# Kernel optimization log

Hardware: AMD Instinct MI355X
Metric: run time of the kernel (lower is better)

Reference implementation:

```python
import jax, jax.numpy as jnp
import numpy as np

WINDOW_SIZE = 11
SIGMA = 1.5
C1 = 0.01 ** 2
C2 = 0.03 ** 2


def _gaussian_window(window_size: int, channel: int) -> jnp.ndarray:
    # 1D gaussian, normalized
    g = jnp.arange(window_size, dtype=jnp.float32) - window_size // 2
    g = jnp.exp(-(g ** 2) / (2.0 * SIGMA ** 2))
    g = g / g.sum()
    w2d = jnp.outer(g, g)  # [K, K]
    # depthwise conv kernel: [C, 1, K, K] in OIHW with feature_group_count=C
    return jnp.broadcast_to(w2d[None, None], (channel, 1, window_size, window_size))


def _depthwise_conv(x: jnp.ndarray, window: jnp.ndarray, channel: int) -> jnp.ndarray:
    pad = WINDOW_SIZE // 2
    return jax.lax.conv_general_dilated(
        x, window,
        window_strides=(1, 1),
        padding=((pad, pad), (pad, pad)),
        dimension_numbers=('NCHW', 'OIHW', 'NCHW'),
        feature_group_count=channel,
    )


def setup_inputs() -> dict:
    key = jax.random.key(0)
    k1, k2 = jax.random.split(key)
    shape = (16, 3, 512, 512)
    img1 = jax.random.uniform(k1, shape, dtype=jnp.float32)
    img2 = jax.random.uniform(k2, shape, dtype=jnp.float32)
    return {"img1": img1, "img2": img2}


def reference(img1, img2):
    channel = img1.shape[1]
    window = _gaussian_window(WINDOW_SIZE, channel).astype(img1.dtype)

    mu1 = _depthwise_conv(img1, window, channel)
    mu2 = _depthwise_conv(img2, window, channel)

    mu1_sq = mu1 * mu1
    mu2_sq = mu2 * mu2
    mu1_mu2 = mu1 * mu2

    sigma1_sq = _depthwise_conv(img1 * img1, window, channel) - mu1_sq
    sigma2_sq = _depthwise_conv(img2 * img2, window, channel) - mu2_sq
    sigma12 = _depthwise_conv(img1 * img2, window, channel) - mu1_mu2

    ssim_map = ((2.0 * mu1_mu2 + C1) * (2.0 * sigma12 + C2)) / (
        (mu1_sq + mu2_sq + C1) * (sigma1_sq + sigma2_sq + C2))

    return 1.0 - ssim_map.mean()
```

## Files before the change

kernel.cpp:

```cpp
#include <hip/hip_runtime.h>

#define IMG_H 512
#define IMG_W 512
#define NPLANES 48
#define N_ELEMS (16 * 3 * 512 * 512)

#define TW 32
#define TH 32
#define NTHREADS 256
#define GX (IMG_W / TW)
#define GY (IMG_H / TH)
#define NBLOCKS (GX * GY * NPLANES)

#define RS4 43

#define C1f 1.0e-4f
#define C2f 9.0e-4f

typedef float v2f __attribute__((ext_vector_type(2)));

__device__ __forceinline__ v2f pkfma(float w, v2f v, v2f acc) {
    v2f wv = {w, w};
    return __builtin_elementwise_fma(wv, v, acc);
}

__global__ void __launch_bounds__(NTHREADS, 7) ssim_main(
    const float* __restrict__ img1, const float* __restrict__ img2,
    float* __restrict__ partials)
{
    __shared__ float4 r[TH * RS4];
    __shared__ float wpart[NTHREADS / 64];

    const int tid = threadIdx.x;

    const int work = (blockIdx.x & 7) * (NBLOCKS / 8) + (blockIdx.x >> 3);
    const int plane = work >> 8;
    const int rem = work & 255;
    const int by = rem >> 4, bx = rem & 15;
    const int tx0 = bx * TW, ty0 = by * TH;
    const float* p1 = img1 + (size_t)plane * IMG_H * IMG_W;
    const float* p2 = img2 + (size_t)plane * IMG_H * IMG_W;

    constexpr float G[11] = {
        0.00102838f, 0.00759876f, 0.03600077f, 0.10936070f, 0.21300553f,
        0.26601173f,
        0.21300553f, 0.10936070f, 0.03600077f, 0.00759876f, 0.00102838f
    };

    if (tid < 168) {
        const int c = tid % 42;
        const int g = tid / 42;
        const int gx = tx0 - 5 + c;
        const int gy0 = ty0 + 8 * g - 5;

        v2f asd[8], ass[8];
#pragma unroll
        for (int k = 0; k < 8; ++k) { asd[k] = (v2f)0.0f; ass[k] = (v2f)0.0f; }

        const bool inter = ((unsigned)gx < IMG_W) & (gy0 >= 0) &
                           (gy0 + 17 < IMG_H);
        if (inter) {
            const float* pa = p1 + (size_t)gy0 * IMG_W + gx;
            const float* pb = p2 + (size_t)gy0 * IMG_W + gx;
#pragma unroll
            for (int j = 0; j < 18; ++j) {
                float a = pa[j * IMG_W];
                float b = pb[j * IMG_W];
                v2f sd; sd.x = a + b; sd.y = a - b;
                v2f sq = sd * sd;
#pragma unroll
                for (int k = 0; k < 8; ++k) {
                    int t = j - k;
                    if (t >= 0 && t < 11) {
                        asd[k] = pkfma(G[t], sd, asd[k]);
                        ass[k] = pkfma(G[t], sq, ass[k]);
                    }
                }
            }
        } else {
            const int cx = min(max(gx, 0), IMG_W - 1);
            const float mx = ((unsigned)gx < IMG_W) ? 1.0f : 0.0f;
#pragma unroll
            for (int j = 0; j < 18; ++j) {
                int gy = gy0 + j;
                int cy = min(max(gy, 0), IMG_H - 1);
                float m = ((unsigned)gy < IMG_H) ? mx : 0.0f;
                size_t off = (size_t)cy * IMG_W + cx;
                float a = p1[off] * m;
                float b = p2[off] * m;
                v2f sd; sd.x = a + b; sd.y = a - b;
                v2f sq = sd * sd;
#pragma unroll
                for (int k = 0; k < 8; ++k) {
                    int t = j - k;
                    if (t >= 0 && t < 11) {
                        asd[k] = pkfma(G[t], sd, asd[k]);
                        ass[k] = pkfma(G[t], sq, ass[k]);
                    }
                }
            }
        }
#pragma unroll
        for (int k = 0; k < 8; ++k)
            r[(8 * g + k) * RS4 + c] =
                make_float4(asd[k].x, asd[k].y, ass[k].x, ass[k].y);
    }
    __syncthreads();

    float local = 0.0f;
    if (tid < 128) {
        const int hy = tid >> 2;
        const int x0 = (tid & 3) * 8;
        v2f osd[8], oss[8];
#pragma unroll
        for (int k = 0; k < 8; ++k) { osd[k] = (v2f)0.0f; oss[k] = (v2f)0.0f; }

#pragma unroll
        for (int j = 0; j < 18; ++j) {
            float4 v = r[hy * RS4 + x0 + j];
            v2f va; va.x = v.x; va.y = v.y;
            v2f vb; vb.x = v.z; vb.y = v.w;
#pragma unroll
            for (int k = 0; k < 8; ++k) {
                int t = j - k;
                if (t >= 0 && t < 11) {
                    osd[k] = pkfma(G[t], va, osd[k]);
                    oss[k] = pkfma(G[t], vb, oss[k]);
                }
            }
        }

#pragma unroll
        for (int k = 0; k < 8; ++k) {
            v2f sd2 = osd[k] * osd[k];
            float cs2 = sd2.x, cd2 = sd2.y;
            float css = oss[k].x, cdd = oss[k].y;
            float mu12 = 0.25f * (cs2 - cd2);
            float musq = 0.50f * (cs2 + cd2);
            float e12  = 0.25f * (css - cdd);
            float esum = 0.50f * (css + cdd);
            float sg12  = e12 - mu12;
            float sgsum = esum - musq;
            float num = (2.0f * mu12 + C1f) * (2.0f * sg12 + C2f);
            float den = (musq + C1f) * (sgsum + C2f);
            local += num * __builtin_amdgcn_rcpf(den);
        }
    }

#pragma unroll
    for (int off = 32; off > 0; off >>= 1) local += __shfl_down(local, off, 64);
    if ((tid & 63) == 0) wpart[tid >> 6] = local;
    __syncthreads();
    if (tid == 0)
        partials[blockIdx.x] = wpart[0] + wpart[1] + wpart[2] + wpart[3];
}

__global__ void ssim_final(const float* __restrict__ partials,
                           float* __restrict__ out)
{
    __shared__ float wp[4];
    const int tid = threadIdx.x;
    const float4* p4 = (const float4*)partials;
    float s = 0.0f;
#pragma unroll
    for (int k = 0; k < 12; ++k) {
        float4 v = p4[tid + k * NTHREADS];
        s += (v.x + v.y) + (v.z + v.w);
    }
#pragma unroll
    for (int off = 32; off > 0; off >>= 1) s += __shfl_down(s, off, 64);
    if ((tid & 63) == 0) wp[tid >> 6] = s;
    __syncthreads();
    if (tid == 0)
        out[0] = 1.0f - (wp[0] + wp[1] + wp[2] + wp[3]) * (1.0f / (float)N_ELEMS);
}

extern "C" void kernel_launch(void* const* d_in, const int* in_sizes, int n_in,
                              void* d_out, int out_size, void* d_ws, size_t ws_size,
                              hipStream_t stream) {
    const float* img1 = (const float*)d_in[0];
    const float* img2 = (const float*)d_in[1];
    float* out = (float*)d_out;
    float* partials = (float*)d_ws;

    ssim_main<<<NBLOCKS, NTHREADS, 0, stream>>>(img1, img2, partials);
    ssim_final<<<1, NTHREADS, 0, stream>>>(partials, out);
}
```

Baseline: 150.2 us.

## Compute separable Gaussian convolutions with bf16 MFMA banded-matrix products

Replaces the scalar packed-FMA separable Gaussian passes with bf16 MFMA 16x16x32 matrix multiplies against banded Gaussian weight matrices. Image sums, differences and their squares are packed to bf16, then run through a horizontal pass. The results go to LDS as transposed bf16, and the vertical pass is a second MFMA. Global loads become vectorized float4 row reads. The aim is to move the convolution arithmetic off the vector ALUs, at the cost of bf16 rounding of inputs, squares and intermediates, which may hurt accuracy of the variance terms.

```diff
diff --git a/kernel.cpp b/kernel.cpp
--- a/kernel.cpp
+++ b/kernel.cpp
@@ -4,152 +4,153 @@
 #define IMG_W 512
 #define NPLANES 48
 #define N_ELEMS (16 * 3 * 512 * 512)
-
-#define TW 32
-#define TH 32
 #define NTHREADS 256
-#define GX (IMG_W / TW)
-#define GY (IMG_H / TH)
-#define NBLOCKS (GX * GY * NPLANES)
-
-#define RS4 43
+#define NBLOCKS 12288
+#define LSTR 56
 
 #define C1f 1.0e-4f
 #define C2f 9.0e-4f
 
-typedef float v2f __attribute__((ext_vector_type(2)));
+typedef float v4f __attribute__((ext_vector_type(4)));
+typedef short v8s __attribute__((ext_vector_type(8)));
 
-__device__ __forceinline__ v2f pkfma(float w, v2f v, v2f acc) {
-    v2f wv = {w, w};
-    return __builtin_elementwise_fma(wv, v, acc);
+__device__ __constant__ float GT[64] = {
+    0,0,0,0,0,0,0,0,0,0,0,0,0,0,0,0,0,0,0,0,0,0,0,0,
+    0.00102838f, 0.00759876f, 0.03600077f, 0.10936070f, 0.21300553f,
+    0.26601173f,
+    0.21300553f, 0.10936070f, 0.03600077f, 0.00759876f, 0.00102838f,
+    0,0,0,0,0,0,0,0,0,0,0,0,0,0,0,0,0,0,0,0,0,0,0,0,0,0,0,0,0
+};
+
+__device__ __forceinline__ unsigned int pk2bf(float x, float y) {
+    unsigned int ax = __float_as_uint(x) + 0x8000u;
+    unsigned int by = __float_as_uint(y) + 0x8000u;
+    return __builtin_amdgcn_perm(by, ax, 0x07060302);
 }
 
-__global__ void __launch_bounds__(NTHREADS, 7) ssim_main(
+__global__ void __launch_bounds__(NTHREADS, 4) ssim_main(
     const float* __restrict__ img1, const float* __restrict__ img2,
     float* __restrict__ partials)
 {
-    __shared__ float4 r[TH * RS4];
-    __shared__ float wpart[NTHREADS / 64];
+    __shared__ short T[128 * LSTR];
+    __shared__ float wpart[4];
 
     const int tid = threadIdx.x;
+    const int lane = tid & 63;
+    const int wv = tid >> 6;
+    const int m = lane & 15;
+    const int qd = lane >> 4;
 
     const int work = (blockIdx.x & 7) * (NBLOCKS / 8) + (blockIdx.x >> 3);
     const int plane = work >> 8;
     const int rem = work & 255;
     const int by = rem >> 4, bx = rem & 15;
-    const int tx0 = bx * TW, ty0 = by * TH;
+    const int tx0 = bx * 32, ty0 = by * 32;
     const float* p1 = img1 + (size_t)plane * IMG_H * IMG_W;
     const float* p2 = img2 + (size_t)plane * IMG_H * IMG_W;
 
-    constexpr float G[11] = {
-        0.00102838f, 0.00759876f, 0.03600077f, 0.10936070f, 0.21300553f,
-        0.26601173f,
-        0.21300553f, 0.10936070f, 0.03600077f, 0.00759876f, 0.00102838f
-    };
+    v8s gX, gY;
+    {
+        union { v8s v; unsigned int u[4]; } uy, ux;
+#pragma unroll
+        for (int i = 0; i < 4; ++i) {
+            int k0 = qd * 8 + 2 * i;
+            uy.u[i] = pk2bf(GT[24 + k0 - m], GT[25 + k0 - m]);
+            ux.u[i] = pk2bf(GT[21 + k0 - m], GT[22 + k0 - m]);
+        }
+        gY = uy.v; gX = ux.v;
+    }
 
-    if (tid < 168) {
-        const int c = tid % 42;
-        const int g = tid / 42;
-        const int gx = tx0 - 5 + c;
-        const int gy0 = ty0 + 8 * g - 5;
+    const bool interior = (bx > 0) & (bx < 15) & (by > 0) & (by < 15);
+    const v4f zero4 = {0.f, 0.f, 0.f, 0.f};
 
-        v2f asd[8], ass[8];
 #pragma unroll
-        for (int k = 0; k < 8; ++k) { asd[k] = (v2f)0.0f; ass[k] = (v2f)0.0f; }
-
-        const bool inter = ((unsigned)gx < IMG_W) & (gy0 >= 0) &
-                           (gy0 + 17 < IMG_H);
-        if (inter) {
-            const float* pa = p1 + (size_t)gy0 * IMG_W + gx;
-            const float* pb = p2 + (size_t)gy0 * IMG_W + gx;
+    for (int cc = 0; cc < 2; ++cc) {
+        int c = wv + 4 * cc;
+        if (c < 6) {
+            const int yg = c >> 1, xoh = c & 1;
+            const int yrow = yg * 16 + m;
+            const int gy = ty0 - 5 + yrow;
+            const int xb = tx0 - 8 + xoh * 16 + qd * 8;
+            float a[8], b[8];
+            if (interior) {
+                const float* pa = p1 + (size_t)gy * IMG_W + xb;
+                const float* pb = p2 + (size_t)gy * IMG_W + xb;
+                *(float4*)&a[0] = *(const float4*)pa;
+                *(float4*)&a[4] = *(const float4*)(pa + 4);
+                *(float4*)&b[0] = *(const float4*)pb;
+                *(float4*)&b[4] = *(const float4*)(pb + 4);
+            } else {
+                const int gyc = min(max(gy, 0), IMG_H - 1);
+                const bool oky = (unsigned)gy < IMG_H;
+                const float* ra = p1 + (size_t)gyc * IMG_W;
+                const float* rb = p2 + (size_t)gyc * IMG_W;
 #pragma unroll
-            for (int j = 0; j < 18; ++j) {
-                float a = pa[j * IMG_W];
-                float b = pb[j * IMG_W];
-                v2f sd; sd.x = a + b; sd.y = a - b;
-                v2f sq = sd * sd;
-#pragma unroll
-                for (int k = 0; k < 8; ++k) {
-                    int t = j - k;
-                    if (t >= 0 && t < 11) {
-                        asd[k] = pkfma(G[t], sd, asd[k]);
-                        ass[k] = pkfma(G[t], sq, ass[k]);
-                    }
+                for (int j = 0; j < 8; ++j) {
+                    int gx = xb + j;
+                    int gxc = min(max(gx, 0), IMG_W - 1);
+                    bool ok = oky && ((unsigned)gx < IMG_W);
+                    a[j] = ok ? ra[gxc] : 0.f;
+                    b[j] = ok ? rb[gxc] : 0.f;
                 }
             }
-        } else {
-            const int cx = min(max(gx, 0), IMG_W - 1);
-            const float mx = ((unsigned)gx < IMG_W) ? 1.0f : 0.0f;
+            union { v8s v; unsigned int u[4]; } fs, fd, fss, fdd;
 #pragma unroll
-            for (int j = 0; j < 18; ++j) {
-                int gy = gy0 + j;
-                int cy = min(max(gy, 0), IMG_H - 1);
-                float m = ((unsigned)gy < IMG_H) ? mx : 0.0f;
-                size_t off = (size_t)cy * IMG_W + cx;
-                float a = p1[off] * m;
-                float b = p2[off] * m;
-                v2f sd; sd.x = a + b; sd.y = a - b;
-                v2f sq = sd * sd;
-#pragma unroll
-                for (int k = 0; k < 8; ++k) {
-                    int t = j - k;
-                    if (t >= 0 && t < 11) {
-                        asd[k] = pkfma(G[t], sd, asd[k]);
-                        ass[k] = pkfma(G[t], sq, ass[k]);
-                    }
-                }
+            for (int i = 0; i < 4; ++i) {
+                float s0 = a[2*i] + b[2*i], s1 = a[2*i+1] + b[2*i+1];
+                float d0 = a[2*i] - b[2*i], d1 = a[2*i+1] - b[2*i+1];
+                fs.u[i]  = pk2bf(s0, s1);
+                fd.u[i]  = pk2bf(d0, d1);
+                fss.u[i] = pk2bf(s0 * s0, s1 * s1);
+                fdd.u[i] = pk2bf(d0 * d0, d1 * d1);
             }
+            v4f t0 = __builtin_amdgcn_mfma_f32_16x16x32_bf16(fs.v,  gX, zero4, 0, 0, 0);
+            v4f t1 = __builtin_amdgcn_mfma_f32_16x16x32_bf16(fd.v,  gX, zero4, 0, 0, 0);
+            v4f t2 = __builtin_amdgcn_mfma_f32_16x16x32_bf16(fss.v, gX, zero4, 0, 0, 0);
+            v4f t3 = __builtin_amdgcn_mfma_f32_16x16x32_bf16(fdd.v, gX, zero4, 0, 0, 0);
+            const int ybase = yg * 16 + qd * 4;
+            const int rbase = xoh * 16 + m;
+            *(uint2*)&T[(0 * 32 + rbase) * LSTR + ybase] =
+                make_uint2(pk2bf(t0[0], t0[1]), pk2bf(t0[2], t0[3]));
+            *(uint2*)&T[(1 * 32 + rbase) * LSTR + ybase] =
+                make_uint2(pk2bf(t1[0], t1[1]), pk2bf(t1[2], t1[3]));
+            *(uint2*)&T[(2 * 32 + rbase) * LSTR + ybase] =
+                make_uint2(pk2bf(t2[0], t2[1]), pk2bf(t2[2], t2[3]));
+            *(uint2*)&T[(3 * 32 + rbase) * LSTR + ybase] =
+                make_uint2(pk2bf(t3[0], t3[1]), pk2bf(t3[2], t3[3]));
         }
-#pragma unroll
-        for (int k = 0; k < 8; ++k)
-            r[(8 * g + k) * RS4 + c] =
-                make_float4(asd[k].x, asd[k].y, ass[k].x, ass[k].y);
     }
     __syncthreads();
 
-    float local = 0.0f;
-    if (tid < 128) {
-        const int hy = tid >> 2;
-        const int x0 = (tid & 3) * 8;
-        v2f osd[8], oss[8];
+    const int yh = wv >> 1, xh = wv & 1;
+    v4f acc[4];
 #pragma unroll
-        for (int k = 0; k < 8; ++k) { osd[k] = (v2f)0.0f; oss[k] = (v2f)0.0f; }
+    for (int q = 0; q < 4; ++q) {
+        const int off = (q * 32 + xh * 16 + m) * LSTR + yh * 16 + qd * 8;
+        v8s tf = *(const v8s*)&T[off];
+        acc[q] = __builtin_amdgcn_mfma_f32_16x16x32_bf16(gY, tf, zero4, 0, 0, 0);
+    }
 
+    float local = 0.f;
 #pragma unroll
-        for (int j = 0; j < 18; ++j) {
-            float4 v = r[hy * RS4 + x0 + j];
-            v2f va; va.x = v.x; va.y = v.y;
-            v2f vb; vb.x = v.z; vb.y = v.w;
-#pragma unroll
-            for (int k = 0; k < 8; ++k) {
-                int t = j - k;
-                if (t >= 0 && t < 11) {
-                    osd[k] = pkfma(G[t], va, osd[k]);
-                    oss[k] = pkfma(G[t], vb, oss[k]);
-                }
-            }
-        }
-
-#pragma unroll
-        for (int k = 0; k < 8; ++k) {
-            v2f sd2 = osd[k] * osd[k];
-            float cs2 = sd2.x, cd2 = sd2.y;
-            float css = oss[k].x, cdd = oss[k].y;
-            float mu12 = 0.25f * (cs2 - cd2);
-            float musq = 0.50f * (cs2 + cd2);
-            float e12  = 0.25f * (css - cdd);
-            float esum = 0.50f * (css + cdd);
-            float sg12  = e12 - mu12;
-            float sgsum = esum - musq;
-            float num = (2.0f * mu12 + C1f) * (2.0f * sg12 + C2f);
-            float den = (musq + C1f) * (sgsum + C2f);
-            local += num * __builtin_amdgcn_rcpf(den);
-        }
+    for (int r = 0; r < 4; ++r) {
+        float cs = acc[0][r], cd = acc[1][r];
+        float css = acc[2][r], cdd = acc[3][r];
+        float cs2 = cs * cs, cd2 = cd * cd;
+        float mu12 = 0.25f * (cs2 - cd2);
+        float musq = 0.50f * (cs2 + cd2);
+        float e12  = 0.25f * (css - cdd);
+        float esum = 0.50f * (css + cdd);
+        float sg12  = e12 - mu12;
+        float sgsum = esum - musq;
+        float num = (2.f * mu12 + C1f) * (2.f * sg12 + C2f);
+        float den = (musq + C1f) * (sgsum + C2f);
+        local += num * __builtin_amdgcn_rcpf(den);
     }
 
 #pragma unroll
     for (int off = 32; off > 0; off >>= 1) local += __shfl_down(local, off, 64);
-    if ((tid & 63) == 0) wpart[tid >> 6] = local;
+    if (lane == 0) wpart[wv] = local;
     __syncthreads();
     if (tid == 0)
         partials[blockIdx.x] = wpart[0] + wpart[1] + wpart[2] + wpart[3];
```

Result: slower. 164.6 us (+9.6%).

## Restructure SSIM into per-wave strips looping over planes with block-free sync

Applied to the files above, without the earlier changes.

Replaces the 32x32 tile per block with per-wavefront strips: each 64-lane wave computes an 8-row by 54-column output strip. The vertical pass is done per lane and the horizontal pass goes through a wave-private LDS region, which removes the block-wide barrier between the two passes. Each wave loops over 6 planes, and the grid is fixed at 1280 blocks mapped to XCDs. This is meant to cut sync, idle threads and launch overhead, at the cost of halo overlap (64 columns loaded for 54 outputs), masked lanes, and a lower occupancy hint.

```diff
diff --git a/kernel.cpp b/kernel.cpp
--- a/kernel.cpp
+++ b/kernel.cpp
@@ -1,18 +1,12 @@
 #include <hip/hip_runtime.h>
 
+#define IMG_W 512
 #define IMG_H 512
-#define IMG_W 512
-#define NPLANES 48
-#define N_ELEMS (16 * 3 * 512 * 512)
-
-#define TW 32
-#define TH 32
+#define PLANE_PX (IMG_W * IMG_H)
+#define N_ELEMS (48 * PLANE_PX)
 #define NTHREADS 256
-#define GX (IMG_W / TW)
-#define GY (IMG_H / TH)
-#define NBLOCKS (GX * GY * NPLANES)
-
-#define RS4 43
+#define NBLK 1280
+#define SPW 6
 
 #define C1f 1.0e-4f
 #define C2f 9.0e-4f
@@ -24,22 +18,11 @@
     return __builtin_elementwise_fma(wv, v, acc);
 }
 
-__global__ void __launch_bounds__(NTHREADS, 7) ssim_main(
+__global__ void __launch_bounds__(NTHREADS, 5) ssim_main(
     const float* __restrict__ img1, const float* __restrict__ img2,
     float* __restrict__ partials)
 {
-    __shared__ float4 r[TH * RS4];
-    __shared__ float wpart[NTHREADS / 64];
-
-    const int tid = threadIdx.x;
-
-    const int work = (blockIdx.x & 7) * (NBLOCKS / 8) + (blockIdx.x >> 3);
-    const int plane = work >> 8;
-    const int rem = work & 255;
-    const int by = rem >> 4, bx = rem & 15;
-    const int tx0 = bx * TW, ty0 = by * TH;
-    const float* p1 = img1 + (size_t)plane * IMG_H * IMG_W;
-    const float* p2 = img2 + (size_t)plane * IMG_H * IMG_W;
+    __shared__ float4 V[2048];
 
     constexpr float G[11] = {
         0.00102838f, 0.00759876f, 0.03600077f, 0.10936070f, 0.21300553f,
@@ -47,112 +30,130 @@
         0.21300553f, 0.10936070f, 0.03600077f, 0.00759876f, 0.00102838f
     };
 
-    if (tid < 168) {
-        const int c = tid % 42;
-        const int g = tid / 42;
-        const int gx = tx0 - 5 + c;
-        const int gy0 = ty0 + 8 * g - 5;
+    const int tid = threadIdx.x;
+    const int lane = tid & 63;
+    const int wv = tid >> 6;
+    float4* Vw = V + wv * 512;
 
-        v2f asd[8], ass[8];
+    const int xcd = blockIdx.x & 7;
+    const int slot = (blockIdx.x >> 3) * 4 + wv;
+    const int band = slot / 10;
+    const int scol = slot - band * 10;
+    const int ry0 = band * 8 - 5;
+    const bool interior = (band >= 1) & (band <= 62);
+
+    const int gx = scol * 54 - 5 + lane;
+    const int cgx = min(max(gx, 0), IMG_W - 1);
+    const float ml = ((unsigned)gx < (unsigned)IMG_W) ? 1.f : 0.f;
+    const v2f mlv = {ml, ml};
+
+    const int kq = lane >> 3;
+    const int cg = lane & 7;
+    const int c0 = cg * 7;
+    const bool cglt7 = (cg < 7);
+
+    float local = 0.f;
+
+    for (int it = 0; it < SPW; ++it) {
+        const int plane = xcd * SPW + it;
+        const float* pa = img1 + (size_t)plane * PLANE_PX + cgx;
+        const float* pb = img2 + (size_t)plane * PLANE_PX + cgx;
+
+        v2f asd[8], asq[8];
 #pragma unroll
-        for (int k = 0; k < 8; ++k) { asd[k] = (v2f)0.0f; ass[k] = (v2f)0.0f; }
+        for (int kk = 0; kk < 8; ++kk) { asd[kk] = (v2f)0.f; asq[kk] = (v2f)0.f; }
 
-        const bool inter = ((unsigned)gx < IMG_W) & (gy0 >= 0) &
-                           (gy0 + 17 < IMG_H);
-        if (inter) {
-            const float* pa = p1 + (size_t)gy0 * IMG_W + gx;
-            const float* pb = p2 + (size_t)gy0 * IMG_W + gx;
+        if (interior) {
 #pragma unroll
             for (int j = 0; j < 18; ++j) {
-                float a = pa[j * IMG_W];
-                float b = pb[j * IMG_W];
+                float a = pa[(ry0 + j) * IMG_W];
+                float b = pb[(ry0 + j) * IMG_W];
                 v2f sd; sd.x = a + b; sd.y = a - b;
                 v2f sq = sd * sd;
 #pragma unroll
-                for (int k = 0; k < 8; ++k) {
-                    int t = j - k;
+                for (int kk = 0; kk < 8; ++kk) {
+                    int t = j - kk;
                     if (t >= 0 && t < 11) {
-                        asd[k] = pkfma(G[t], sd, asd[k]);
-                        ass[k] = pkfma(G[t], sq, ass[k]);
+                        asd[kk] = pkfma(G[t], sd, asd[kk]);
+                        asq[kk] = pkfma(G[t], sq, asq[kk]);
                     }
                 }
             }
         } else {
-            const int cx = min(max(gx, 0), IMG_W - 1);
-            const float mx = ((unsigned)gx < IMG_W) ? 1.0f : 0.0f;
 #pragma unroll
             for (int j = 0; j < 18; ++j) {
-                int gy = gy0 + j;
-                int cy = min(max(gy, 0), IMG_H - 1);
-                float m = ((unsigned)gy < IMG_H) ? mx : 0.0f;
-                size_t off = (size_t)cy * IMG_W + cx;
-                float a = p1[off] * m;
-                float b = p2[off] * m;
+                int ry = ry0 + j;
+                int ryc = min(max(ry, 0), IMG_H - 1);
+                float rm = ((unsigned)ry < (unsigned)IMG_H) ? 1.f : 0.f;
+                float a = pa[ryc * IMG_W] * rm;
+                float b = pb[ryc * IMG_W] * rm;
                 v2f sd; sd.x = a + b; sd.y = a - b;
                 v2f sq = sd * sd;
 #pragma unroll
-                for (int k = 0; k < 8; ++k) {
-                    int t = j - k;
+                for (int kk = 0; kk < 8; ++kk) {
+                    int t = j - kk;
                     if (t >= 0 && t < 11) {
-                        asd[k] = pkfma(G[t], sd, asd[k]);
-                        ass[k] = pkfma(G[t], sq, ass[k]);
+                        asd[kk] = pkfma(G[t], sd, asd[kk]);
+                        asq[kk] = pkfma(G[t], sq, asq[kk]);
                     }
-                }
-            }
-        }
-#pragma unroll
-        for (int k = 0; k < 8; ++k)
-            r[(8 * g + k) * RS4 + c] =
-                make_float4(asd[k].x, asd[k].y, ass[k].x, ass[k].y);
-    }
-    __syncthreads();
-
-    float local = 0.0f;
-    if (tid < 128) {
-        const int hy = tid >> 2;
-        const int x0 = (tid & 3) * 8;
-        v2f osd[8], oss[8];
-#pragma unroll
-        for (int k = 0; k < 8; ++k) { osd[k] = (v2f)0.0f; oss[k] = (v2f)0.0f; }
-
-#pragma unroll
-        for (int j = 0; j < 18; ++j) {
-            float4 v = r[hy * RS4 + x0 + j];
-            v2f va; va.x = v.x; va.y = v.y;
-            v2f vb; vb.x = v.z; vb.y = v.w;
-#pragma unroll
-            for (int k = 0; k < 8; ++k) {
-                int t = j - k;
-                if (t >= 0 && t < 11) {
-                    osd[k] = pkfma(G[t], va, osd[k]);
-                    oss[k] = pkfma(G[t], vb, oss[k]);
                 }
             }
         }
 
 #pragma unroll
-        for (int k = 0; k < 8; ++k) {
-            v2f sd2 = osd[k] * osd[k];
-            float cs2 = sd2.x, cd2 = sd2.y;
-            float css = oss[k].x, cdd = oss[k].y;
+        for (int kk = 0; kk < 8; ++kk) {
+            v2f wsd = asd[kk] * mlv;
+            v2f wsq = asq[kk] * mlv;
+            Vw[kk * 64 + lane] = make_float4(wsd.x, wsd.y, wsq.x, wsq.y);
+        }
+
+        v2f osd[7], osq[7];
+#pragma unroll
+        for (int o = 0; o < 7; ++o) { osd[o] = (v2f)0.f; osq[o] = (v2f)0.f; }
+
+        const float4* row = Vw + kq * 64;
+#pragma unroll
+        for (int j = 0; j < 17; ++j) {
+            int cidx = (j < 15) ? (c0 + j) : min(c0 + j, 63);
+            float4 v = row[cidx];
+            v2f vsd; vsd.x = v.x; vsd.y = v.y;
+            v2f vsq; vsq.x = v.z; vsq.y = v.w;
+#pragma unroll
+            for (int o = 0; o < 7; ++o) {
+                int t = j - o;
+                if (t >= 0 && t < 11) {
+                    osd[o] = pkfma(G[t], vsd, osd[o]);
+                    osq[o] = pkfma(G[t], vsq, osq[o]);
+                }
+            }
+        }
+
+        const int gxo0 = scol * 54 + c0;
+#pragma unroll
+        for (int o = 0; o < 7; ++o) {
+            v2f s2 = osd[o] * osd[o];
+            float cs2 = s2.x, cd2 = s2.y;
+            float css = osq[o].x, cdd = osq[o].y;
             float mu12 = 0.25f * (cs2 - cd2);
             float musq = 0.50f * (cs2 + cd2);
             float e12  = 0.25f * (css - cdd);
             float esum = 0.50f * (css + cdd);
-            float sg12  = e12 - mu12;
-            float sgsum = esum - musq;
-            float num = (2.0f * mu12 + C1f) * (2.0f * sg12 + C2f);
-            float den = (musq + C1f) * (sgsum + C2f);
-            local += num * __builtin_amdgcn_rcpf(den);
+            float num = (2.f * mu12 + C1f) * (2.f * (e12 - mu12) + C2f);
+            float den = (musq + C1f) * ((esum - musq) + C2f);
+            float sv = num * __builtin_amdgcn_rcpf(den);
+            bool valid = (gxo0 + o < IMG_W) && (o < 5 || cglt7);
+            local += valid ? sv : 0.f;
         }
     }
 
 #pragma unroll
     for (int off = 32; off > 0; off >>= 1) local += __shfl_down(local, off, 64);
-    if ((tid & 63) == 0) wpart[tid >> 6] = local;
+    if (lane == 0) ((float*)Vw)[0] = local;
     __syncthreads();
-    if (tid == 0)
-        partials[blockIdx.x] = wpart[0] + wpart[1] + wpart[2] + wpart[3];
+    if (tid == 0) {
+        const float* Vf = (const float*)V;
+        partials[blockIdx.x] = Vf[0] + Vf[2048] + Vf[4096] + Vf[6144];
+    }
 }
 
 __global__ void ssim_final(const float* __restrict__ partials,
@@ -161,10 +162,9 @@
     __shared__ float wp[4];
     const int tid = threadIdx.x;
     const float4* p4 = (const float4*)partials;
-    float s = 0.0f;
-#pragma unroll
-    for (int k = 0; k < 12; ++k) {
-        float4 v = p4[tid + k * NTHREADS];
+    float s = 0.f;
+    for (int i = tid; i < NBLK / 4; i += NTHREADS) {
+        float4 v = p4[i];
         s += (v.x + v.y) + (v.z + v.w);
     }
 #pragma unroll
@@ -183,6 +183,6 @@
     float* out = (float*)d_out;
     float* partials = (float*)d_ws;
 
-    ssim_main<<<NBLOCKS, NTHREADS, 0, stream>>>(img1, img2, partials);
+    ssim_main<<<NBLK, NTHREADS, 0, stream>>>(img1, img2, partials);
     ssim_final<<<1, NTHREADS, 0, stream>>>(partials, out);
 }
```

Result: slower. 275.1 us (+83.2%).
